# Performance work log

Measured on AMD Instinct MI355X. Metric: run time of the kernel, lower is better.

## Reference

```python
import jax, jax.numpy as jnp
import numpy as np

NUM_HEADS = 16
DIM_HEAD = 64
DIM = 1024
SCALE = DIM ** (-0.5)  # NOTE: source scales by model dim, not dim_head


def setup_inputs() -> dict:
    key = jax.random.key(0)
    ks = jax.random.split(key, 6)
    b, n, d = 2, 2048, DIM
    return {
        "x": jax.random.normal(ks[0], (b, n, d), dtype=jnp.float32),
        "mask": jnp.ones((b, n), dtype=bool),
        "Wq": jax.random.normal(ks[1], (NUM_HEADS * DIM_HEAD, d), dtype=jnp.float32) * 0.02,
        "Wk": jax.random.normal(ks[2], (DIM_HEAD, d), dtype=jnp.float32) * 0.02,
        "Wv": jax.random.normal(ks[3], (DIM_HEAD, d), dtype=jnp.float32) * 0.02,
        "Wfc": jax.random.normal(ks[4], (d, NUM_HEADS * DIM_HEAD), dtype=jnp.float32) * 0.02,
        "bfc": jnp.zeros((d,), dtype=jnp.float32),
    }


def reference(x, mask, Wq, Wk, Wv, Wfc, bfc):
    b, n, _ = x.shape
    # projections (nn.Linear: y = x @ W.T)
    q = (x @ Wq.T).reshape(b, n, NUM_HEADS, DIM_HEAD).transpose(0, 2, 1, 3)  # b h n d
    k = x @ Wk.T  # b n d  (single shared MQA head)
    v = x @ Wv.T  # b n d
    energy = jnp.einsum("bhid,bjd->bhij", q, k) * SCALE  # b h i j
    mask_value = -jnp.finfo(energy.dtype).max
    # input mask: k_mask is all ones in source, so only query rows are masked
    q_mask = mask[:, None, :, None]  # b 1 i 1
    energy = jnp.where(q_mask, energy, mask_value)
    # causal mask: positions j > i are masked (i == j since self-attention)
    i = jnp.arange(n)
    causal = i[:, None] < i[None, :]  # True where future
    energy = jnp.where(causal[None, None, :, :], mask_value, energy)
    attn = jax.nn.softmax(energy, axis=-1)
    # dropout_rate = 0.0 -> identity
    out = jnp.einsum("bhij,bjd->bhid", attn, v)
    out = out.transpose(0, 2, 1, 3).reshape(b, n, NUM_HEADS * DIM_HEAD)
    return out @ Wfc.T + bfc
```

## Files before the change

kernel.cpp:

```cpp
#include <hip/hip_runtime.h>
#include <math.h>

#define NH 16
#define DH 64
#define DM 1024
#define NS 2048
#define BB 2
#define MR (BB * NS)
#define LDQ 1152
#define C_EXP 0.0450842201f

typedef unsigned short u16;
typedef __attribute__((ext_vector_type(8))) short short8;
typedef __attribute__((ext_vector_type(4))) short short4v;
typedef __attribute__((ext_vector_type(4))) float floatx4;
typedef __attribute__((ext_vector_type(4))) u16 u16x4;

#if __has_builtin(__builtin_amdgcn_exp2f)
#define EXP2(x) __builtin_amdgcn_exp2f(x)
#else
#define EXP2(x) exp2f(x)
#endif

#define MFMA16(a, b, c) __builtin_amdgcn_mfma_f32_16x16x32_bf16((a), (b), (c), 0, 0, 0)

#if __has_builtin(__builtin_amdgcn_mfma_f32_16x16x16bf16_1k)
#define MFMAK16(a, b, c) __builtin_amdgcn_mfma_f32_16x16x16bf16_1k((a), (b), (c), 0, 0, 0)
#else
static __device__ __forceinline__ floatx4 mfmak16_(short4v a, short4v b, floatx4 c) {
  asm("v_mfma_f32_16x16x16_bf16 %0, %1, %2, %0" : "+v"(c) : "v"(a), "v"(b));
  return c;
}
#define MFMAK16(a, b, c) mfmak16_((a), (b), (c))
#endif

static __device__ __forceinline__ u16 f2bf(float f) {
  union { float f; unsigned u; } v; v.f = f;
  unsigned r = v.u + 0x7fffu + ((v.u >> 16) & 1u);
  return (u16)(r >> 16);
}
static __device__ __forceinline__ u16 f2bf_fast(float f) {
  union { float f; unsigned u; } v; v.f = f;
  return (u16)((v.u + 0x8000u) >> 16);
}

#define GLDS16(gp, lp)                                                        \
  __builtin_amdgcn_global_load_lds(                                           \
      (const __attribute__((address_space(1))) void*)(const void*)(gp),       \
      (__attribute__((address_space(3))) void*)(void*)(lp), 16, 0, 0)

__global__ __launch_bounds__(256) void cast_all(
    const float* __restrict__ x, const float* __restrict__ wq,
    const float* __restrict__ wk, const float* __restrict__ wv,
    const float* __restrict__ wfc, u16* __restrict__ xb,
    u16* __restrict__ wqkvb, u16* __restrict__ wfcb) {
  const int NX = MR * DM / 4, NQ = DM * DM / 4, NK = DH * DM / 4;
  int id = blockIdx.x * 256 + threadIdx.x;
  const float* src;
  u16* dst;
  int off;
  if (id < NX) { src = x; dst = xb; off = id; }
  else if (id < NX + NQ) { src = wq; dst = wqkvb; off = id - NX; }
  else if (id < NX + NQ + NK) { src = wk; dst = wqkvb + (size_t)DM * DM; off = id - NX - NQ; }
  else if (id < NX + NQ + 2 * NK) { src = wv; dst = wqkvb + (size_t)(DM + DH) * DM; off = id - NX - NQ - NK; }
  else { src = wfc; dst = wfcb; off = id - NX - NQ - 2 * NK; }
  float4 f = ((const float4*)src)[off];
  u16x4 o;
  o[0] = f2bf(f.x); o[1] = f2bf(f.y); o[2] = f2bf(f.z); o[3] = f2bf(f.w);
  ((u16x4*)dst)[off] = o;
}

__global__ __launch_bounds__(256) void gemm64(
    const u16* __restrict__ A, const u16* __restrict__ W,
    const float* __restrict__ bias, void* __restrict__ Cout,
    u16* __restrict__ vT, int M, int N, int K, int ldc, int out_bf16,
    int v_by) {
  __shared__ u16 As[2][64 * 32];
  __shared__ u16 Ws[2][64 * 32];
  const int tid = threadIdx.x;
  const int lane = tid & 63;
  const int lr = lane & 15, quad = lane >> 4;
  const int wave = tid >> 6, wr = wave >> 1, wc = wave & 1;

  const int lin = blockIdx.y * gridDim.x + blockIdx.x;
  const int xcd = lin & 7, slot = lin >> 3;
  const int bx = xcd * 8 + (slot & 7), by = slot >> 3;
  const int m0 = bx * 64, n0 = by * 64;

  const int srow = tid >> 2;
  const int scg = (tid & 3) ^ ((srow >> 1) & 3);
  const u16* gA = A + (size_t)(m0 + srow) * K + scg * 8;
  const u16* gW = W + (size_t)(n0 + srow) * K + scg * 8;
  const int lo = wave * 512;

  floatx4 acc[2][2] = {};
  const int nt = K >> 5;

  GLDS16(gA, &As[0][lo]);
  GLDS16(gW, &Ws[0][lo]);

  for (int t = 0; t < nt; ++t) {
    __syncthreads();
    if (t + 1 < nt) {
      const int ko = (t + 1) << 5;
      const int nb = (t + 1) & 1;
      GLDS16(gA + ko, &As[nb][lo]);
      GLDS16(gW + ko, &Ws[nb][lo]);
    }
    const u16* as = As[t & 1];
    const u16* ws = Ws[t & 1];
    short8 af[2], wf[2];
#pragma unroll
    for (int mi = 0; mi < 2; ++mi) {
      int rr = wr * 32 + mi * 16 + lr;
      af[mi] = *(const short8*)&as[rr * 32 + ((quad ^ ((rr >> 1) & 3)) << 3)];
    }
#pragma unroll
    for (int nj = 0; nj < 2; ++nj) {
      int rc = wc * 32 + nj * 16 + lr;
      wf[nj] = *(const short8*)&ws[rc * 32 + ((quad ^ ((rc >> 1) & 3)) << 3)];
    }
#pragma unroll
    for (int mi = 0; mi < 2; ++mi)
#pragma unroll
      for (int nj = 0; nj < 2; ++nj)
        acc[mi][nj] = MFMA16(af[mi], wf[nj], acc[mi][nj]);
  }

  if (v_by >= 0 && by == v_by) {
#pragma unroll
    for (int mi = 0; mi < 2; ++mi)
#pragma unroll
      for (int nj = 0; nj < 2; ++nj)
#pragma unroll
        for (int r = 0; r < 4; ++r)
          vT[(size_t)(wc * 32 + nj * 16 + lr) * MR + m0 + wr * 32 + mi * 16 +
             quad * 4 + r] = f2bf(acc[mi][nj][r]);
    return;
  }

#pragma unroll
  for (int mi = 0; mi < 2; ++mi) {
#pragma unroll
    for (int nj = 0; nj < 2; ++nj) {
      int col = n0 + wc * 32 + nj * 16 + lr;
      float badd = bias ? bias[col] : 0.f;
#pragma unroll
      for (int r = 0; r < 4; ++r) {
        int row = m0 + wr * 32 + mi * 16 + quad * 4 + r;
        float v = acc[mi][nj][r] + badd;
        if (out_bf16)
          ((u16*)Cout)[(size_t)row * ldc + col] = f2bf(v);
        else
          ((float*)Cout)[(size_t)row * ldc + col] = v;
      }
    }
  }
}

__global__ __launch_bounds__(512) void attn_mfma(
    const u16* __restrict__ qkv,
    const u16* __restrict__ vT,
    u16* __restrict__ aob) {
  __shared__ __align__(16) u16 smem[4 * 8192];

  const int b = blockIdx.z;
  const int p = blockIdx.x;
  const int tid = threadIdx.x;
  const int lane = tid & 63;
  const int lr = lane & 15, quad = lane >> 4;
  const int w = tid >> 6;
  const int hl = w & 3;
  const int half = w >> 2;
  const int head = blockIdx.y * 4 + hl;
  const int hb = half * 64;
  const size_t rowb = (size_t)b * NS;
  const u16* kvK = qkv + rowb * LDQ + 1024;
  const u16* vTb = vT + rowb;

  int skrow[2], skcg[2], svrow[2], svcg[2], lo[2];
#pragma unroll
  for (int g = 0; g < 2; ++g) {
    const int ci = g * 512 + tid;
    skrow[g] = ci >> 3;
    skcg[g] = (ci & 7) ^ (skrow[g] & 7);
    svrow[g] = ci >> 4;
    svcg[g] = (ci & 15) ^ (svrow[g] & 15);
    lo[g] = (g * 512 + w * 64) * 8;
  }

  for (int phase = 0; phase < 2; ++phase) {
    const int s = (phase == 0) ? (63 - p) : p;
    const int i0q = s * 32;
    const int ntp = (s >> 2) + 1;
    const int irowA = i0q + lr;
    const int irowB = i0q + 16 + lr;

    const u16* qpA = qkv + (rowb + i0q + lr) * LDQ + head * DH;
    const u16* qpB = qpA + 16 * LDQ;
    short8 aqA0 = *(const short8*)(qpA + quad * 8);
    short8 aqA1 = *(const short8*)(qpA + 32 + quad * 8);
    short8 aqB0 = *(const short8*)(qpB + quad * 8);
    short8 aqB1 = *(const short8*)(qpB + 32 + quad * 8);

    floatx4 oA[4] = {}, oB[4] = {};
    float laccA = 0.f, laccB = 0.f;

    __syncthreads();
#pragma unroll
    for (int g = 0; g < 2; ++g) {
      GLDS16(kvK + (size_t)skrow[g] * LDQ + skcg[g] * 8, &smem[lo[g]]);
      GLDS16(vTb + (size_t)svrow[g] * MR + svcg[g] * 8, &smem[16384 + lo[g]]);
    }

    for (int t = 0; t < ntp; ++t) {
      const int buf = t & 1;
      __syncthreads();

      if (t + 1 < ntp) {
        const int j0n = (t + 1) * 128;
        const int nb2 = (buf ^ 1) * 8192;
#pragma unroll
        for (int g = 0; g < 2; ++g) {
          GLDS16(kvK + (size_t)(j0n + skrow[g]) * LDQ + skcg[g] * 8,
                 &smem[nb2 + lo[g]]);
          GLDS16(vTb + (size_t)svrow[g] * MR + j0n + svcg[g] * 8,
                 &smem[16384 + nb2 + lo[g]]);
        }
      }

      const int j0 = t * 128;
      const u16* ksb = smem + buf * 8192;
      const u16* vtb = smem + 16384 + buf * 8192;
      const bool lastt = (t == ntp - 1);

      if (lastt && half == 1 && (s & 3) < 2) continue;

#pragma unroll
      for (int jb = 0; jb < 4; ++jb) {
        const int krow = hb + jb * 16 + lr;
        short8 bk0 = *(const short8*)&ksb[krow * 64 + ((quad ^ (krow & 7)) << 3)];
        short8 bk1 = *(const short8*)&ksb[krow * 64 + (((4 + quad) ^ (krow & 7)) << 3)];
        floatx4 zA = {}, zB = {};
        zA = MFMA16(bk0, aqA0, zA);
        zA = MFMA16(bk1, aqA1, zA);
        zB = MFMA16(bk0, aqB0, zB);
        zB = MFMA16(bk1, aqB1, zB);

        const int kbase = j0 + hb + jb * 16 + (quad << 2);
        short4v apA, apB;
#pragma unroll
        for (int r = 0; r < 4; ++r) {
          float peA = EXP2(zA[r] * C_EXP);
          float peB = EXP2(zB[r] * C_EXP);
          if (lastt && (kbase + r > irowA)) peA = 0.f;
          if (lastt && (kbase + r > irowB)) peB = 0.f;
          laccA += peA;
          laccB += peB;
          apA[r] = (short)f2bf_fast(peA);
          apB[r] = (short)f2bf_fast(peB);
        }

#pragma unroll
        for (int nb = 0; nb < 4; ++nb) {
          const int d = nb * 16 + lr;
          const int va = d * 128 +
                         (((8 * half + 2 * jb + (quad >> 1)) ^ (d & 15)) << 3) +
                         ((quad & 1) << 2);
          short4v bv = *(const short4v*)&vtb[va];
          oA[nb] = MFMAK16(apA, bv, oA[nb]);
          oB[nb] = MFMAK16(apB, bv, oB[nb]);
        }
      }
    }

    laccA += __shfl_xor(laccA, 16);
    laccA += __shfl_xor(laccA, 32);
    laccB += __shfl_xor(laccB, 16);
    laccB += __shfl_xor(laccB, 32);

    __syncthreads();
    float* M = (float*)smem;
    float* Mh = M + hl * 34 * 64;
    if (half == 1) {
#pragma unroll
      for (int nb = 0; nb < 4; ++nb)
#pragma unroll
        for (int r = 0; r < 4; ++r) {
          Mh[(nb * 4 + r) * 64 + lane] = oA[nb][r];
          Mh[(16 + nb * 4 + r) * 64 + lane] = oB[nb][r];
        }
      Mh[32 * 64 + lane] = laccA;
      Mh[33 * 64 + lane] = laccB;
    }
    __syncthreads();
    if (half == 0) {
#pragma unroll
      for (int nb = 0; nb < 4; ++nb)
#pragma unroll
        for (int r = 0; r < 4; ++r) {
          oA[nb][r] += Mh[(nb * 4 + r) * 64 + lane];
          oB[nb][r] += Mh[(16 + nb * 4 + r) * 64 + lane];
        }
      laccA += Mh[32 * 64 + lane];
      laccB += Mh[33 * 64 + lane];

      float dA[4], dB[4];
#pragma unroll
      for (int r = 0; r < 4; ++r) {
        dA[r] = __shfl(laccA, (quad << 2) + r);
        dB[r] = __shfl(laccB, (quad << 2) + r);
      }
#pragma unroll
      for (int nb = 0; nb < 4; ++nb)
#pragma unroll
        for (int r = 0; r < 4; ++r) {
          const int col = head * DH + nb * 16 + lr;
          aob[(rowb + i0q + (quad << 2) + r) * DM + col] =
              f2bf(oA[nb][r] / dA[r]);
          aob[(rowb + i0q + 16 + (quad << 2) + r) * DM + col] =
              f2bf(oB[nb][r] / dB[r]);
        }
    }
  }
}

extern "C" void kernel_launch(void* const* d_in, const int* in_sizes, int n_in,
                              void* d_out, int out_size, void* d_ws, size_t ws_size,
                              hipStream_t stream) {
  const float* x = (const float*)d_in[0];
  const float* Wq = (const float*)d_in[2];
  const float* Wk = (const float*)d_in[3];
  const float* Wv = (const float*)d_in[4];
  const float* Wfc = (const float*)d_in[5];
  const float* bfc = (const float*)d_in[6];

  u16* xb = (u16*)d_ws;
  u16* wqkvb = xb + (size_t)MR * DM;
  u16* wfcb = wqkvb + (size_t)LDQ * DM;
  u16* qkv = wfcb + (size_t)DM * DM;
  u16* vT = qkv + (size_t)MR * LDQ;
  u16* aob = xb;

  cast_all<<<dim3((MR * DM + DM * DM * 2 + DH * DM * 2) / 1024), dim3(256), 0,
             stream>>>(x, Wq, Wk, Wv, Wfc, xb, wqkvb, wfcb);
  gemm64<<<dim3(MR / 64, LDQ / 64), dim3(256), 0, stream>>>(
      xb, wqkvb, nullptr, qkv, vT, MR, LDQ, DM, LDQ, 1, 17);
  attn_mfma<<<dim3(32, NH / 4, BB), dim3(512), 0, stream>>>(qkv, vT, aob);
  gemm64<<<dim3(MR / 64, DM / 64), dim3(256), 0, stream>>>(
      aob, wfcb, bfc, d_out, nullptr, MR, DM, DM, DM, 0, -1);
}
```

Before: 152.9 us.

## Fuse x fp32-to-bf16 cast into QKV GEMM loads and add MFMA priority hints

Removes the x cast from the cast kernel. The QKV GEMM now reads fp32 x directly, converts it to bf16 in registers and stores it to LDS, which saves a full bf16 round-trip of x through memory. The attention kernel raises wave priority around its MFMA groups and loads all V fragments before issuing the PV MFMAs. In exchange, the fused A-load path is a synchronous register load instead of an async global-to-LDS load, which may stall the GEMM pipeline.

```diff
diff --git a/kernel.cpp b/kernel.cpp
--- a/kernel.cpp
+++ b/kernel.cpp
@@ -15,6 +15,7 @@
 typedef __attribute__((ext_vector_type(4))) short short4v;
 typedef __attribute__((ext_vector_type(4))) float floatx4;
 typedef __attribute__((ext_vector_type(4))) u16 u16x4;
+typedef __attribute__((ext_vector_type(8))) u16 u16x8;
 
 #if __has_builtin(__builtin_amdgcn_exp2f)
 #define EXP2(x) __builtin_amdgcn_exp2f(x)
@@ -50,20 +51,18 @@
       (__attribute__((address_space(3))) void*)(void*)(lp), 16, 0, 0)
 
 __global__ __launch_bounds__(256) void cast_all(
-    const float* __restrict__ x, const float* __restrict__ wq,
-    const float* __restrict__ wk, const float* __restrict__ wv,
-    const float* __restrict__ wfc, u16* __restrict__ xb,
+    const float* __restrict__ wq, const float* __restrict__ wk,
+    const float* __restrict__ wv, const float* __restrict__ wfc,
     u16* __restrict__ wqkvb, u16* __restrict__ wfcb) {
-  const int NX = MR * DM / 4, NQ = DM * DM / 4, NK = DH * DM / 4;
+  const int NQ = DM * DM / 4, NK = DH * DM / 4;
   int id = blockIdx.x * 256 + threadIdx.x;
   const float* src;
   u16* dst;
   int off;
-  if (id < NX) { src = x; dst = xb; off = id; }
-  else if (id < NX + NQ) { src = wq; dst = wqkvb; off = id - NX; }
-  else if (id < NX + NQ + NK) { src = wk; dst = wqkvb + (size_t)DM * DM; off = id - NX - NQ; }
-  else if (id < NX + NQ + 2 * NK) { src = wv; dst = wqkvb + (size_t)(DM + DH) * DM; off = id - NX - NQ - NK; }
-  else { src = wfc; dst = wfcb; off = id - NX - NQ - 2 * NK; }
+  if (id < NQ) { src = wq; dst = wqkvb; off = id; }
+  else if (id < NQ + NK) { src = wk; dst = wqkvb + (size_t)DM * DM; off = id - NQ; }
+  else if (id < NQ + 2 * NK) { src = wv; dst = wqkvb + (size_t)(DM + DH) * DM; off = id - NQ - NK; }
+  else { src = wfc; dst = wfcb; off = id - NQ - 2 * NK; }
   float4 f = ((const float4*)src)[off];
   u16x4 o;
   o[0] = f2bf(f.x); o[1] = f2bf(f.y); o[2] = f2bf(f.z); o[3] = f2bf(f.w);
@@ -71,10 +70,10 @@
 }
 
 __global__ __launch_bounds__(256) void gemm64(
-    const u16* __restrict__ A, const u16* __restrict__ W,
+    const void* __restrict__ A, const u16* __restrict__ W,
     const float* __restrict__ bias, void* __restrict__ Cout,
     u16* __restrict__ vT, int M, int N, int K, int ldc, int out_bf16,
-    int v_by) {
+    int v_by, int a_fp32) {
   __shared__ u16 As[2][64 * 32];
   __shared__ u16 Ws[2][64 * 32];
   const int tid = threadIdx.x;
@@ -89,14 +88,24 @@
 
   const int srow = tid >> 2;
   const int scg = (tid & 3) ^ ((srow >> 1) & 3);
-  const u16* gA = A + (size_t)(m0 + srow) * K + scg * 8;
+  const u16* gA16 = (const u16*)A + (size_t)(m0 + srow) * K + scg * 8;
+  const float* gAf = (const float*)A + (size_t)(m0 + srow) * K + scg * 8;
   const u16* gW = W + (size_t)(n0 + srow) * K + scg * 8;
   const int lo = wave * 512;
 
   floatx4 acc[2][2] = {};
   const int nt = K >> 5;
 
-  GLDS16(gA, &As[0][lo]);
+  if (a_fp32) {
+    float4 u = *(const float4*)(gAf);
+    float4 v = *(const float4*)(gAf + 4);
+    u16x8 o;
+    o[0] = f2bf(u.x); o[1] = f2bf(u.y); o[2] = f2bf(u.z); o[3] = f2bf(u.w);
+    o[4] = f2bf(v.x); o[5] = f2bf(v.y); o[6] = f2bf(v.z); o[7] = f2bf(v.w);
+    *(u16x8*)&As[0][lo + lane * 8] = o;
+  } else {
+    GLDS16(gA16, &As[0][lo]);
+  }
   GLDS16(gW, &Ws[0][lo]);
 
   for (int t = 0; t < nt; ++t) {
@@ -104,7 +113,16 @@
     if (t + 1 < nt) {
       const int ko = (t + 1) << 5;
       const int nb = (t + 1) & 1;
-      GLDS16(gA + ko, &As[nb][lo]);
+      if (a_fp32) {
+        float4 u = *(const float4*)(gAf + ko);
+        float4 v = *(const float4*)(gAf + ko + 4);
+        u16x8 o;
+        o[0] = f2bf(u.x); o[1] = f2bf(u.y); o[2] = f2bf(u.z); o[3] = f2bf(u.w);
+        o[4] = f2bf(v.x); o[5] = f2bf(v.y); o[6] = f2bf(v.z); o[7] = f2bf(v.w);
+        *(u16x8*)&As[nb][lo + lane * 8] = o;
+      } else {
+        GLDS16(gA16 + ko, &As[nb][lo]);
+      }
       GLDS16(gW + ko, &Ws[nb][lo]);
     }
     const u16* as = As[t & 1];
@@ -242,10 +260,12 @@
         short8 bk0 = *(const short8*)&ksb[krow * 64 + ((quad ^ (krow & 7)) << 3)];
         short8 bk1 = *(const short8*)&ksb[krow * 64 + (((4 + quad) ^ (krow & 7)) << 3)];
         floatx4 zA = {}, zB = {};
+        __builtin_amdgcn_s_setprio(1);
         zA = MFMA16(bk0, aqA0, zA);
         zA = MFMA16(bk1, aqA1, zA);
         zB = MFMA16(bk0, aqB0, zB);
         zB = MFMA16(bk1, aqB1, zB);
+        __builtin_amdgcn_s_setprio(0);
 
         const int kbase = j0 + hb + jb * 16 + (quad << 2);
         short4v apA, apB;
@@ -261,16 +281,22 @@
           apB[r] = (short)f2bf_fast(peB);
         }
 
+        short4v bvv[4];
 #pragma unroll
         for (int nb = 0; nb < 4; ++nb) {
           const int d = nb * 16 + lr;
           const int va = d * 128 +
                          (((8 * half + 2 * jb + (quad >> 1)) ^ (d & 15)) << 3) +
                          ((quad & 1) << 2);
-          short4v bv = *(const short4v*)&vtb[va];
-          oA[nb] = MFMAK16(apA, bv, oA[nb]);
-          oB[nb] = MFMAK16(apB, bv, oB[nb]);
-        }
+          bvv[nb] = *(const short4v*)&vtb[va];
+        }
+        __builtin_amdgcn_s_setprio(1);
+#pragma unroll
+        for (int nb = 0; nb < 4; ++nb) {
+          oA[nb] = MFMAK16(apA, bvv[nb], oA[nb]);
+          oB[nb] = MFMAK16(apB, bvv[nb], oB[nb]);
+        }
+        __builtin_amdgcn_s_setprio(0);
       }
     }
 
@@ -335,18 +361,17 @@
   const float* Wfc = (const float*)d_in[5];
   const float* bfc = (const float*)d_in[6];
 
-  u16* xb = (u16*)d_ws;
-  u16* wqkvb = xb + (size_t)MR * DM;
+  u16* aob = (u16*)d_ws;
+  u16* wqkvb = aob + (size_t)MR * DM;
   u16* wfcb = wqkvb + (size_t)LDQ * DM;
   u16* qkv = wfcb + (size_t)DM * DM;
   u16* vT = qkv + (size_t)MR * LDQ;
-  u16* aob = xb;
-
-  cast_all<<<dim3((MR * DM + DM * DM * 2 + DH * DM * 2) / 1024), dim3(256), 0,
-             stream>>>(x, Wq, Wk, Wv, Wfc, xb, wqkvb, wfcb);
+
+  cast_all<<<dim3((DM * DM * 2 + DH * DM * 2) / 1024), dim3(256), 0, stream>>>(
+      Wq, Wk, Wv, Wfc, wqkvb, wfcb);
   gemm64<<<dim3(MR / 64, LDQ / 64), dim3(256), 0, stream>>>(
-      xb, wqkvb, nullptr, qkv, vT, MR, LDQ, DM, LDQ, 1, 17);
+      x, wqkvb, nullptr, qkv, vT, MR, LDQ, DM, LDQ, 1, 17, 1);
   attn_mfma<<<dim3(32, NH / 4, BB), dim3(512), 0, stream>>>(qkv, vT, aob);
   gemm64<<<dim3(MR / 64, DM / 64), dim3(256), 0, stream>>>(
-      aob, wfcb, bfc, d_out, nullptr, MR, DM, DM, DM, 0, -1);
-}
+      aob, wfcb, bfc, d_out, nullptr, MR, DM, DM, DM, 0, -1, 0);
+}
```

After: 158.1 us. 3.4% more time.
